# Optimization experiments

Hardware: AMD Instinct MI355X
Metric: run time of the kernel (lower is better)

## Reference

```python
import jax, jax.numpy as jnp
import numpy as np

H = 1024
NH = 16
HD = H // NH
EPS = 1e-5


def _layernorm(x, g, b):
    mu = jnp.mean(x, axis=-1, keepdims=True)
    var = jnp.mean((x - mu) ** 2, axis=-1, keepdims=True)
    return (x - mu) * jax.lax.rsqrt(var + EPS) * g + b


def setup_inputs() -> dict:
    key = jax.random.key(0)
    ks = jax.random.split(key, 12)
    s = lambda fan_in: 1.0 / np.sqrt(fan_in)
    x = jax.random.normal(ks[0], (2, 2048, H), dtype=jnp.float32)
    return {
        "x": x,
        "ln1_g": jnp.ones((H,), jnp.float32),
        "ln1_b": jnp.zeros((H,), jnp.float32),
        "W_qkv": jax.random.uniform(ks[1], (H, 3 * H), jnp.float32, -s(H), s(H)),
        "b_qkv": jax.random.uniform(ks[2], (3 * H,), jnp.float32, -s(H), s(H)),
        "W_out": jax.random.uniform(ks[3], (H, H), jnp.float32, -s(H), s(H)),
        "b_out": jax.random.uniform(ks[4], (H,), jnp.float32, -s(H), s(H)),
        "ln2_g": jnp.ones((H,), jnp.float32),
        "ln2_b": jnp.zeros((H,), jnp.float32),
        "W1": jax.random.uniform(ks[5], (H, 4 * H), jnp.float32, -s(H), s(H)),
        "b1": jax.random.uniform(ks[6], (4 * H,), jnp.float32, -s(H), s(H)),
        "W2": jax.random.uniform(ks[7], (4 * H, H), jnp.float32, -s(4 * H), s(4 * H)),
        "b2": jax.random.uniform(ks[8], (H,), jnp.float32, -s(4 * H), s(4 * H)),
    }


def reference(x, ln1_g, ln1_b, W_qkv, b_qkv, W_out, b_out, ln2_g, ln2_b, W1, b1, W2, b2):
    B, S, _ = x.shape
    residual = x
    h = _layernorm(x, ln1_g, ln1_b)
    qkv = h @ W_qkv + b_qkv                     # [B,S,3H]
    qkv = qkv.reshape(B, S, 3, NH, HD)
    q, k, v = qkv[:, :, 0], qkv[:, :, 1], qkv[:, :, 2]  # [B,S,NH,HD]
    scale = 1.0 / np.sqrt(HD)
    attn = jnp.einsum("bqhd,bkhd->bhqk", q, k) * scale  # [B,NH,S,S]
    attn = jax.nn.softmax(attn, axis=-1)
    out = jnp.einsum("bhqk,bkhd->bqhd", attn, v).reshape(B, S, H)
    x = residual + (out @ W_out + b_out)
    residual = x
    h = _layernorm(x, ln2_g, ln2_b)
    h = jax.nn.gelu(h @ W1 + b1, approximate=False) @ W2 + b2
    return residual + h
```

## Files before the change

### kernel.cpp

```cpp
#include <hip/hip_runtime.h>
#include <hip/hip_bf16.h>
#include <math.h>

#define HDIM 1024
#define SEQ  2048
#define BATCH 2
#define NHEAD 16
#define HEADD 64

typedef short bf16x8 __attribute__((ext_vector_type(8)));
typedef float f32x4  __attribute__((ext_vector_type(4)));
typedef unsigned short u16x8 __attribute__((ext_vector_type(8)));
typedef unsigned short u16x4 __attribute__((ext_vector_type(4)));

__device__ __forceinline__ unsigned short f2bf(float f) {
    unsigned u = __float_as_uint(f);
    unsigned r = (u + 0x7FFFu + ((u >> 16) & 1u)) >> 16;
    return (unsigned short)r;
}
__device__ __forceinline__ float b2f(unsigned short s) {
    return __uint_as_float(((unsigned)s) << 16);
}
__device__ __forceinline__ unsigned pk2bf(float lo, float hi) {
    __hip_bfloat162 h = __float22bfloat162_rn(float2{lo, hi});
    unsigned r;
    __builtin_memcpy(&r, &h, 4);
    return r;
}
__device__ __forceinline__ float fexp2(float x) {
#if __has_builtin(__builtin_amdgcn_exp2f)
    return __builtin_amdgcn_exp2f(x);
#else
    return exp2f(x);
#endif
}
__device__ __forceinline__ void gld16(void* lds, const void* g) {
    __builtin_amdgcn_global_load_lds(
        (const __attribute__((address_space(1))) unsigned int*)(g),
        (__attribute__((address_space(3))) unsigned int*)(lds),
        16, 0, 0);
}

#define SWZ(row, chunk) (((row) * 64) + (((chunk) ^ ((row) & 7)) << 3))

__global__ __launch_bounds__(256) void ln_kernel(const float* __restrict__ x,
                                                 const float* __restrict__ gw,
                                                 const float* __restrict__ bw,
                                                 unsigned short* __restrict__ y)
{
    int row = blockIdx.x;
    int t = threadIdx.x;
    const float* xr = x + (size_t)row * HDIM;
    float4 v = *(const float4*)(xr + t * 4);
    float s1 = v.x + v.y + v.z + v.w;
    float s2 = v.x * v.x + v.y * v.y + v.z * v.z + v.w * v.w;
#pragma unroll
    for (int m = 1; m < 64; m <<= 1) {
        s1 += __shfl_xor(s1, m);
        s2 += __shfl_xor(s2, m);
    }
    __shared__ float red[8];
    int wid = t >> 6;
    if ((t & 63) == 0) { red[wid * 2] = s1; red[wid * 2 + 1] = s2; }
    __syncthreads();
    if (t == 0) {
        float a = red[0] + red[2] + red[4] + red[6];
        float b = red[1] + red[3] + red[5] + red[7];
        red[0] = a; red[1] = b;
    }
    __syncthreads();
    float mu  = red[0] * (1.0f / HDIM);
    float var = red[1] * (1.0f / HDIM) - mu * mu;
    float rs  = rsqrtf(var + 1e-5f);
    float4 g4 = *(const float4*)(gw + t * 4);
    float4 b4 = *(const float4*)(bw + t * 4);
    ushort4 o;
    o.x = f2bf((v.x - mu) * rs * g4.x + b4.x);
    o.y = f2bf((v.y - mu) * rs * g4.y + b4.y);
    o.z = f2bf((v.z - mu) * rs * g4.z + b4.z);
    o.w = f2bf((v.w - mu) * rs * g4.w + b4.w);
    *(ushort4*)(y + (size_t)row * HDIM + t * 4) = o;
}

__global__ __launch_bounds__(256) void wconv_all(const float* __restrict__ Wq,
                                                 const float* __restrict__ Wo,
                                                 const float* __restrict__ W1,
                                                 const float* __restrict__ W2,
                                                 unsigned short* __restrict__ WqT,
                                                 unsigned short* __restrict__ WoT,
                                                 unsigned short* __restrict__ W1T,
                                                 unsigned short* __restrict__ W2T)
{
    int bid = blockIdx.x;
    const float* W; unsigned short* WT; int K, nx, idx;
    if (bid < 3072)      { W = Wq; WT = WqT; K = 1024; nx = 96;  idx = bid; }
    else if (bid < 4096) { W = Wo; WT = WoT; K = 1024; nx = 32;  idx = bid - 3072; }
    else if (bid < 8192) { W = W1; WT = W1T; K = 1024; nx = 128; idx = bid - 4096; }
    else                 { W = W2; WT = W2T; K = 4096; nx = 32;  idx = bid - 8192; }
    int N = nx * 32;
    int n0 = (idx % nx) * 32, k0 = (idx / nx) * 32;

    __shared__ float tile[32][33];
    int t = threadIdx.x, c = t & 31, r = t >> 5;
#pragma unroll
    for (int i = 0; i < 4; ++i)
        tile[r + 8 * i][c] = W[(size_t)(k0 + r + 8 * i) * N + n0 + c];
    __syncthreads();
#pragma unroll
    for (int i = 0; i < 4; ++i)
        WT[(size_t)(n0 + r + 8 * i) * K + k0 + c] = f2bf(tile[c][r + 8 * i]);
}

template <int EPI>
__global__ __launch_bounds__(256, 2) void mgemm(const unsigned short* __restrict__ A,
                                                const unsigned short* __restrict__ BT,
                                                const float* __restrict__ bias,
                                                const float* __restrict__ resid,
                                                float* __restrict__ Cf,
                                                unsigned short* __restrict__ Cb,
                                                int M, int N, int K)
{
    __shared__ char smem[65536];
    int t = threadIdx.x;
    int bn = blockIdx.x * 128, bm = blockIdx.y * 128;
    int l = t & 63, w = t >> 6;
    int wm = w >> 1, wn = w & 1;
    int lrow = l & 15, kq = l >> 4;

    f32x4 acc[4][4];
#pragma unroll
    for (int i = 0; i < 4; ++i)
#pragma unroll
        for (int j = 0; j < 4; ++j) acc[i][j] = {0.f, 0.f, 0.f, 0.f};

    const unsigned short* Ap[4];
    const unsigned short* Bp[4];
    int ld[4];
#pragma unroll
    for (int i = 0; i < 4; ++i) {
        int cid = i * 256 + t;
        int row = cid >> 3, c = cid & 7;
        int gc = (c ^ (row & 7)) << 3;
        Ap[i] = A + (size_t)(bm + row) * K + gc;
        Bp[i] = BT + (size_t)(bn + row) * K + gc;
        ld[i] = cid << 4;
    }

    int nt = K >> 6;
#pragma unroll
    for (int i = 0; i < 4; ++i) {
        gld16(smem + ld[i], Ap[i]);
        gld16(smem + 16384 + ld[i], Bp[i]);
    }
    __syncthreads();

    for (int tk = 0; tk < nt; ++tk) {
        int cur = (tk & 1) << 15;
        if (tk + 1 < nt) {
            int k0 = (tk + 1) << 6;
            int nxt = 32768 - cur;
#pragma unroll
            for (int i = 0; i < 4; ++i) {
                gld16(smem + nxt + ld[i], Ap[i] + k0);
                gld16(smem + nxt + 16384 + ld[i], Bp[i] + k0);
            }
        }
        const unsigned short* sA = (const unsigned short*)(smem + cur);
        const unsigned short* sB = (const unsigned short*)(smem + cur + 16384);
#pragma unroll
        for (int kk = 0; kk < 2; ++kk) {
            bf16x8 af[4], bv[4];
#pragma unroll
            for (int mi = 0; mi < 4; ++mi)
                af[mi] = *(const bf16x8*)(sA + SWZ(wm * 64 + mi * 16 + lrow, kk * 4 + kq));
#pragma unroll
            for (int ni = 0; ni < 4; ++ni)
                bv[ni] = *(const bf16x8*)(sB + SWZ(wn * 64 + ni * 16 + lrow, kk * 4 + kq));
#pragma unroll
            for (int mi = 0; mi < 4; ++mi)
#pragma unroll
                for (int ni = 0; ni < 4; ++ni)
                    acc[mi][ni] = __builtin_amdgcn_mfma_f32_16x16x32_bf16(af[mi], bv[ni], acc[mi][ni], 0, 0, 0);
        }
        __syncthreads();
    }

    int crow = (l >> 4) * 4;
    int ccol = l & 15;
#pragma unroll
    for (int mi = 0; mi < 4; ++mi) {
#pragma unroll
        for (int ni = 0; ni < 4; ++ni) {
            int gcol = bn + wn * 64 + ni * 16 + ccol;
            float bv = bias[gcol];
#pragma unroll
            for (int r = 0; r < 4; ++r) {
                int grow = bm + wm * 64 + mi * 16 + crow + r;
                size_t off = (size_t)grow * N + gcol;
                float v = acc[mi][ni][r] + bv;
                if (EPI == 1) {
                    Cf[off] = v + resid[off];
                } else if (EPI == 2) {
                    v = 0.5f * v * (1.0f + erff(v * 0.70710678118654752f));
                    Cb[off] = f2bf(v);
                } else {
                    Cb[off] = f2bf(v);
                }
            }
        }
    }
}

__global__ __launch_bounds__(512) void mattn(const unsigned short* __restrict__ qkv,
                                             unsigned short* __restrict__ out)
{
    __shared__ unsigned short Qs[128 * 64];
    __shared__ unsigned short Ks[2][64 * 64];
    __shared__ unsigned short Vt[2][64 * 64];
    __shared__ unsigned short Ps[8 * 16 * 64];
    int t = threadIdx.x;
    int w = t >> 6, l = t & 63;
    int lr = l & 15, lh = l >> 4;
    int q0 = blockIdx.x * 128;
    int hh = blockIdx.y, b = blockIdx.z;
    const unsigned short* Qg = qkv + (size_t)b * SEQ * 3072 + hh * 64;
    const unsigned short* Kg = Qg + 1024;
    const unsigned short* Vg = Qg + 2048;

#pragma unroll
    for (int i = 0; i < 2; ++i) {
        int chunkid = i * 512 + t;
        int row = chunkid >> 3, c = chunkid & 7;
        gld16(((char*)Qs) + chunkid * 16,
              Qg + (size_t)(q0 + row) * 3072 + ((c ^ (row & 7)) << 3));
    }

    int kr0 = t >> 3, kc0 = t & 7;
    const unsigned short* Kp0 = Kg + (size_t)kr0 * 3072 + kc0 * 8;
    int kd0 = SWZ(kr0, kc0);
    int vk = (t & 31) * 2;
    int vd0 = ((t >> 5) & 15) * 4;
    const unsigned short* Vp0 = Vg + (size_t)vk * 3072 + vd0;
    const unsigned short* Vp1 = Vp0 + 3072;

    u16x8 k0 = *(const u16x8*)Kp0;
    u16x4 v0 = *(const u16x4*)Vp0;
    u16x4 v1 = *(const u16x4*)Vp1;
    Kp0 += 64 * 3072; Vp0 += 64 * 3072; Vp1 += 64 * 3072;

    __syncthreads();
    bf16x8 qa[2];
#pragma unroll
    for (int ks = 0; ks < 2; ++ks)
        qa[ks] = *(const bf16x8*)(Qs + SWZ(w * 16 + lr, ks * 4 + lh));

    *(u16x8*)(Ks[0] + kd0) = k0;
#pragma unroll
    for (int j = 0; j < 4; ++j) {
        int d = vd0 + j;
        unsigned pack = (unsigned)(unsigned short)v0[j] | ((unsigned)(unsigned short)v1[j] << 16);
        *(unsigned*)(Vt[0] + SWZ(d, vk >> 3) + (vk & 7)) = pack;
    }
    k0 = *(const u16x8*)Kp0;
    v0 = *(const u16x4*)Vp0; v1 = *(const u16x4*)Vp1;
    Kp0 += 64 * 3072; Vp0 += 64 * 3072; Vp1 += 64 * 3072;
    asm volatile("s_waitcnt lgkmcnt(0)" ::: "memory");
    __builtin_amdgcn_s_barrier();

    f32x4 o[4];
#pragma unroll
    for (int i = 0; i < 4; ++i) o[i] = {0.f, 0.f, 0.f, 0.f};
    float mr = -3.0e38f, lsum = 0.f;
    unsigned short* Pw = Ps + w * (16 * 64);
    const float C = 0.18033688011112042f;

    const int nt = SEQ / 64;
    for (int tt = 0; tt < nt; ++tt) {
        const unsigned short* Kc = Ks[tt & 1];
        const unsigned short* Vc = Vt[tt & 1];

        f32x4 s[4];
#pragma unroll
        for (int ni = 0; ni < 4; ++ni) s[ni] = {0.f, 0.f, 0.f, 0.f};
#pragma unroll
        for (int ks = 0; ks < 2; ++ks) {
#pragma unroll
            for (int ni = 0; ni < 4; ++ni) {
                bf16x8 kb = *(const bf16x8*)(Kc + SWZ(ni * 16 + lr, ks * 4 + lh));
                s[ni] = __builtin_amdgcn_mfma_f32_16x16x32_bf16(kb, qa[ks], s[ni], 0, 0, 0);
            }
        }
        float mx = s[0][0];
#pragma unroll
        for (int ni = 0; ni < 4; ++ni)
#pragma unroll
            for (int r = 0; r < 4; ++r) mx = fmaxf(mx, s[ni][r]);
        mx = fmaxf(mx, __shfl_xor(mx, 16));
        mx = fmaxf(mx, __shfl_xor(mx, 32));
        if (__any(mx > mr + 64.0f)) {
            float mn = fmaxf(mr, mx);
            float corr = fexp2((mr - mn) * C);
            mr = mn;
            lsum *= corr;
            float cr[4];
#pragma unroll
            for (int r = 0; r < 4; ++r) cr[r] = __shfl(corr, lh * 4 + r, 16);
#pragma unroll
            for (int nd = 0; nd < 4; ++nd) {
                o[nd][0] *= cr[0]; o[nd][1] *= cr[1];
                o[nd][2] *= cr[2]; o[nd][3] *= cr[3];
            }
        }
        float mc = mr * C;
        float rsum = 0.f;
#pragma unroll
        for (int ni = 0; ni < 4; ++ni)
#pragma unroll
            for (int r = 0; r < 4; ++r) {
                float p = fexp2(fmaf(s[ni][r], C, -mc));
                s[ni][r] = p;
                rsum += p;
            }
        rsum += __shfl_xor(rsum, 16);
        rsum += __shfl_xor(rsum, 32);
        lsum += rsum;
#pragma unroll
        for (int ni = 0; ni < 4; ++ni)
#pragma unroll
            for (int rp = 0; rp < 2; ++rp) {
                int k = ni * 16 + lh * 4 + rp * 2;
                *(unsigned*)(Pw + SWZ(lr, k >> 3) + (k & 7)) =
                    pk2bf(s[ni][rp * 2], s[ni][rp * 2 + 1]);
            }
#pragma unroll
        for (int ks = 0; ks < 2; ++ks) {
            bf16x8 pa = *(const bf16x8*)(Pw + SWZ(lr, ks * 4 + lh));
#pragma unroll
            for (int nd = 0; nd < 4; ++nd) {
                bf16x8 vb = *(const bf16x8*)(Vc + SWZ(nd * 16 + lr, ks * 4 + lh));
                o[nd] = __builtin_amdgcn_mfma_f32_16x16x32_bf16(pa, vb, o[nd], 0, 0, 0);
            }
        }

        if (tt + 1 < nt) {
            int nb = (tt & 1) ^ 1;
            *(u16x8*)(Ks[nb] + kd0) = k0;
#pragma unroll
            for (int j = 0; j < 4; ++j) {
                int d = vd0 + j;
                unsigned pack = (unsigned)(unsigned short)v0[j] | ((unsigned)(unsigned short)v1[j] << 16);
                *(unsigned*)(Vt[nb] + SWZ(d, vk >> 3) + (vk & 7)) = pack;
            }
            if (tt + 2 < nt) {
                k0 = *(const u16x8*)Kp0;
                v0 = *(const u16x4*)Vp0; v1 = *(const u16x4*)Vp1;
                Kp0 += 64 * 3072; Vp0 += 64 * 3072; Vp1 += 64 * 3072;
            }
            asm volatile("s_waitcnt lgkmcnt(0)" ::: "memory");
            __builtin_amdgcn_s_barrier();
        }
    }
    float inv = 1.0f / lsum;
    float ir[4];
#pragma unroll
    for (int r = 0; r < 4; ++r) ir[r] = __shfl(inv, lh * 4 + r, 16);
#pragma unroll
    for (int r = 0; r < 4; ++r) {
        int q = q0 + w * 16 + lh * 4 + r;
#pragma unroll
        for (int nd = 0; nd < 4; ++nd) {
            int d = nd * 16 + lr;
            out[(size_t)((size_t)b * SEQ + q) * HDIM + hh * 64 + d] = f2bf(o[nd][r] * ir[r]);
        }
    }
}

extern "C" void kernel_launch(void* const* d_in, const int* in_sizes, int n_in,
                              void* d_out, int out_size, void* d_ws, size_t ws_size,
                              hipStream_t stream)
{
    const float* x     = (const float*)d_in[0];
    const float* ln1_g = (const float*)d_in[1];
    const float* ln1_b = (const float*)d_in[2];
    const float* W_qkv = (const float*)d_in[3];
    const float* b_qkv = (const float*)d_in[4];
    const float* W_out = (const float*)d_in[5];
    const float* b_out = (const float*)d_in[6];
    const float* ln2_g = (const float*)d_in[7];
    const float* ln2_b = (const float*)d_in[8];
    const float* W1    = (const float*)d_in[9];
    const float* b1    = (const float*)d_in[10];
    const float* W2    = (const float*)d_in[11];
    const float* b2    = (const float*)d_in[12];
    float* out = (float*)d_out;
    char* ws8  = (char*)d_ws;

    const int M = BATCH * SEQ;
    const size_t MB = 1048576;

    unsigned short* hbuf = (unsigned short*)(ws8);
    unsigned short* qkvb = (unsigned short*)(ws8 + 8 * MB);
    unsigned short* attb = (unsigned short*)(ws8 + 32 * MB);
    unsigned short* ffn1 = (unsigned short*)(ws8 + 8 * MB);
    unsigned short* WqT  = (unsigned short*)(ws8 + 40 * MB);
    unsigned short* WoT  = (unsigned short*)(ws8 + 46 * MB);
    unsigned short* W1T  = (unsigned short*)(ws8 + 48 * MB);
    unsigned short* W2T  = (unsigned short*)(ws8 + 56 * MB);

    wconv_all<<<12288, 256, 0, stream>>>(W_qkv, W_out, W1, W2, WqT, WoT, W1T, W2T);

    ln_kernel<<<M, 256, 0, stream>>>(x, ln1_g, ln1_b, hbuf);
    mgemm<0><<<dim3(3 * HDIM / 128, M / 128), 256, 0, stream>>>(hbuf, WqT, b_qkv, nullptr, nullptr, qkvb, M, 3 * HDIM, HDIM);
    mattn<<<dim3(SEQ / 128, NHEAD, BATCH), 512, 0, stream>>>(qkvb, attb);
    mgemm<1><<<dim3(HDIM / 128, M / 128), 256, 0, stream>>>(attb, WoT, b_out, x, out, nullptr, M, HDIM, HDIM);
    ln_kernel<<<M, 256, 0, stream>>>(out, ln2_g, ln2_b, hbuf);
    mgemm<2><<<dim3(4 * HDIM / 128, M / 128), 256, 0, stream>>>(hbuf, W1T, b1, nullptr, nullptr, ffn1, M, 4 * HDIM, HDIM);
    mgemm<1><<<dim3(HDIM / 128, M / 128), 256, 0, stream>>>(ffn1, W2T, b2, out, out, nullptr, M, HDIM, 4 * HDIM);
}
```

Baseline: 232.3 us.

## Add 64-row GEMM tile for N=1024 GEMMs and XCD-aware block remapping

Adds an mgemm64 variant with 64x128 tiles, used for the two output projections whose N is 1024. This doubles the block count from 256 to 512 so all CUs on the MI355X get work. Also remaps workgroup ids so neighbouring tiles land on the same XCD, which should improve L2 reuse in every GEMM. The cost is more total A/B reloads per output element and smaller per-wave MFMA tiles in the new kernel.

```diff
diff --git a/kernel.cpp b/kernel.cpp
--- a/kernel.cpp
+++ b/kernel.cpp
@@ -42,6 +42,14 @@
 }
 
 #define SWZ(row, chunk) (((row) * 64) + (((chunk) ^ ((row) & 7)) << 3))
+
+__device__ __forceinline__ void xcd_remap(int& bx, int& by) {
+    int nx = gridDim.x, nwg = nx * gridDim.y;
+    int hwid = by * nx + bx;
+    int lid = (hwid & 7) * (nwg >> 3) + (hwid >> 3);
+    bx = lid % nx;
+    by = lid / nx;
+}
 
 __global__ __launch_bounds__(256) void ln_kernel(const float* __restrict__ x,
                                                  const float* __restrict__ gw,
@@ -122,7 +130,9 @@
 {
     __shared__ char smem[65536];
     int t = threadIdx.x;
-    int bn = blockIdx.x * 128, bm = blockIdx.y * 128;
+    int bx = blockIdx.x, by = blockIdx.y;
+    xcd_remap(bx, by);
+    int bn = bx * 128, bm = by * 128;
     int l = t & 63, w = t >> 6;
     int wm = w >> 1, wn = w & 1;
     int lrow = l & 15, kq = l >> 4;
@@ -196,6 +206,111 @@
 #pragma unroll
             for (int r = 0; r < 4; ++r) {
                 int grow = bm + wm * 64 + mi * 16 + crow + r;
+                size_t off = (size_t)grow * N + gcol;
+                float v = acc[mi][ni][r] + bv;
+                if (EPI == 1) {
+                    Cf[off] = v + resid[off];
+                } else if (EPI == 2) {
+                    v = 0.5f * v * (1.0f + erff(v * 0.70710678118654752f));
+                    Cb[off] = f2bf(v);
+                } else {
+                    Cb[off] = f2bf(v);
+                }
+            }
+        }
+    }
+}
+
+template <int EPI>
+__global__ __launch_bounds__(256, 2) void mgemm64(const unsigned short* __restrict__ A,
+                                                  const unsigned short* __restrict__ BT,
+                                                  const float* __restrict__ bias,
+                                                  const float* __restrict__ resid,
+                                                  float* __restrict__ Cf,
+                                                  unsigned short* __restrict__ Cb,
+                                                  int M, int N, int K)
+{
+    __shared__ char smem[49152];
+    int t = threadIdx.x;
+    int bx = blockIdx.x, by = blockIdx.y;
+    xcd_remap(bx, by);
+    int bn = bx * 128, bm = by * 64;
+    int l = t & 63, w = t >> 6;
+    int lrow = l & 15, kq = l >> 4;
+
+    f32x4 acc[4][2];
+#pragma unroll
+    for (int i = 0; i < 4; ++i)
+#pragma unroll
+        for (int j = 0; j < 2; ++j) acc[i][j] = {0.f, 0.f, 0.f, 0.f};
+
+    const unsigned short* Ap[2];
+    int ldA[2];
+#pragma unroll
+    for (int i = 0; i < 2; ++i) {
+        int cid = i * 256 + t;
+        int row = cid >> 3, c = cid & 7;
+        Ap[i] = A + (size_t)(bm + row) * K + ((c ^ (row & 7)) << 3);
+        ldA[i] = cid << 4;
+    }
+    const unsigned short* Bp[4];
+    int ldB[4];
+#pragma unroll
+    for (int i = 0; i < 4; ++i) {
+        int cid = i * 256 + t;
+        int row = cid >> 3, c = cid & 7;
+        Bp[i] = BT + (size_t)(bn + row) * K + ((c ^ (row & 7)) << 3);
+        ldB[i] = cid << 4;
+    }
+
+    int nt = K >> 6;
+#pragma unroll
+    for (int i = 0; i < 2; ++i) gld16(smem + ldA[i], Ap[i]);
+#pragma unroll
+    for (int i = 0; i < 4; ++i) gld16(smem + 8192 + ldB[i], Bp[i]);
+    __syncthreads();
+
+    for (int tk = 0; tk < nt; ++tk) {
+        int cur = (tk & 1) * 24576;
+        if (tk + 1 < nt) {
+            int k0 = (tk + 1) << 6;
+            int nxt = 24576 - cur;
+#pragma unroll
+            for (int i = 0; i < 2; ++i) gld16(smem + nxt + ldA[i], Ap[i] + k0);
+#pragma unroll
+            for (int i = 0; i < 4; ++i) gld16(smem + nxt + 8192 + ldB[i], Bp[i] + k0);
+        }
+        const unsigned short* sA = (const unsigned short*)(smem + cur);
+        const unsigned short* sB = (const unsigned short*)(smem + cur + 8192);
+#pragma unroll
+        for (int kk = 0; kk < 2; ++kk) {
+            bf16x8 af[4], bv[2];
+#pragma unroll
+            for (int mi = 0; mi < 4; ++mi)
+                af[mi] = *(const bf16x8*)(sA + SWZ(mi * 16 + lrow, kk * 4 + kq));
+#pragma unroll
+            for (int ni = 0; ni < 2; ++ni)
+                bv[ni] = *(const bf16x8*)(sB + SWZ(w * 32 + ni * 16 + lrow, kk * 4 + kq));
+#pragma unroll
+            for (int mi = 0; mi < 4; ++mi)
+#pragma unroll
+                for (int ni = 0; ni < 2; ++ni)
+                    acc[mi][ni] = __builtin_amdgcn_mfma_f32_16x16x32_bf16(af[mi], bv[ni], acc[mi][ni], 0, 0, 0);
+        }
+        __syncthreads();
+    }
+
+    int crow = (l >> 4) * 4;
+    int ccol = l & 15;
+#pragma unroll
+    for (int mi = 0; mi < 4; ++mi) {
+#pragma unroll
+        for (int ni = 0; ni < 2; ++ni) {
+            int gcol = bn + w * 32 + ni * 16 + ccol;
+            float bv = bias[gcol];
+#pragma unroll
+            for (int r = 0; r < 4; ++r) {
+                int grow = bm + mi * 16 + crow + r;
                 size_t off = (size_t)grow * N + gcol;
                 float v = acc[mi][ni][r] + bv;
                 if (EPI == 1) {
@@ -412,8 +527,8 @@
     ln_kernel<<<M, 256, 0, stream>>>(x, ln1_g, ln1_b, hbuf);
     mgemm<0><<<dim3(3 * HDIM / 128, M / 128), 256, 0, stream>>>(hbuf, WqT, b_qkv, nullptr, nullptr, qkvb, M, 3 * HDIM, HDIM);
     mattn<<<dim3(SEQ / 128, NHEAD, BATCH), 512, 0, stream>>>(qkvb, attb);
-    mgemm<1><<<dim3(HDIM / 128, M / 128), 256, 0, stream>>>(attb, WoT, b_out, x, out, nullptr, M, HDIM, HDIM);
+    mgemm64<1><<<dim3(HDIM / 128, M / 64), 256, 0, stream>>>(attb, WoT, b_out, x, out, nullptr, M, HDIM, HDIM);
     ln_kernel<<<M, 256, 0, stream>>>(out, ln2_g, ln2_b, hbuf);
     mgemm<2><<<dim3(4 * HDIM / 128, M / 128), 256, 0, stream>>>(hbuf, W1T, b1, nullptr, nullptr, ffn1, M, 4 * HDIM, HDIM);
-    mgemm<1><<<dim3(HDIM / 128, M / 128), 256, 0, stream>>>(ffn1, W2T, b2, out, out, nullptr, M, HDIM, 4 * HDIM);
-}
+    mgemm64<1><<<dim3(HDIM / 128, M / 64), 256, 0, stream>>>(ffn1, W2T, b2, out, out, nullptr, M, HDIM, 4 * HDIM);
+}
```

Measured after the change: 226.2 us. 1.03x faster.
